# Kernel optimization log

Hardware: AMD Instinct MI355X
Metric: run time of the kernel (lower is better)

## Reference

```python
import jax, jax.numpy as jnp
import numpy as np

B, S, H, OUT = 4096, 200, 512, 64


def setup_inputs() -> dict:
    key = jax.random.key(0)
    ks = jax.random.split(key, 16)
    sc = 0.05
    return {
        "last_input": jax.random.normal(ks[0], (B, OUT), jnp.float32),
        "hidden": jax.random.normal(ks[1], (1, B, H), jnp.float32),
        "encoder_outputs": jax.random.normal(ks[2], (S, B, H), jnp.float32),
        "attn_W": jax.random.normal(ks[3], (S, H + OUT), jnp.float32) * sc,
        "attn_b": jax.random.normal(ks[4], (S,), jnp.float32) * sc,
        "comb_W": jax.random.normal(ks[5], (H, H + OUT), jnp.float32) * sc,
        "comb_b": jax.random.normal(ks[6], (H,), jnp.float32) * sc,
        "w_ih": jax.random.normal(ks[7], (3 * H, H), jnp.float32) * sc,
        "w_hh": jax.random.normal(ks[8], (3 * H, H), jnp.float32) * sc,
        "b_ih": jax.random.normal(ks[9], (3 * H,), jnp.float32) * sc,
        "b_hh": jax.random.normal(ks[10], (3 * H,), jnp.float32) * sc,
        "out_W": jax.random.normal(ks[11], (OUT, H), jnp.float32) * sc,
        "out_b": jax.random.normal(ks[12], (OUT,), jnp.float32) * sc,
    }


def reference(last_input, hidden, encoder_outputs, attn_W, attn_b, comb_W,
              comb_b, w_ih, w_hh, b_ih, b_hh, out_W, out_b):
    h0 = hidden[0]  # [B,H]
    # Bahdanau-style attention scores over the encoder sequence
    cat1 = jnp.concatenate([last_input, h0], axis=1)          # [B, OUT+H]
    attn_weights = jax.nn.softmax(cat1 @ attn_W.T + attn_b, axis=1)  # [B,S]
    enc = jnp.transpose(encoder_outputs, (1, 0, 2))            # [B,S,H]
    attn_applied = jnp.einsum('bs,bsh->bh', attn_weights, enc)  # [B,H]
    # combine + relu
    cat2 = jnp.concatenate([last_input, attn_applied], axis=1)  # [B, OUT+H]
    x = jax.nn.relu(cat2 @ comb_W.T + comb_b)                   # [B,H]
    # single-step GRU (PyTorch gate order: r, z, n)
    gi = x @ w_ih.T + b_ih                                      # [B,3H]
    gh = h0 @ w_hh.T + b_hh                                     # [B,3H]
    i_r, i_z, i_n = jnp.split(gi, 3, axis=1)
    h_r, h_z, h_n = jnp.split(gh, 3, axis=1)
    r = jax.nn.sigmoid(i_r + h_r)
    z = jax.nn.sigmoid(i_z + h_z)
    n = jnp.tanh(i_n + r * h_n)
    h_new = (1.0 - z) * n + z * h0                              # [B,H]
    out = h_new @ out_W.T + out_b                               # [B,OUT]
    return out, h_new[None], attn_weights
```

## Files before the change

kernel.cpp:

```cpp
#include <hip/hip_runtime.h>
#include <cstddef>

constexpr int Bn = 4096;
constexpr int Sn = 200;
constexpr int Hn = 512;
constexpr int On = 64;
constexpr int K1 = 576;

constexpr size_t HNEW_OFF = (size_t)Bn * On;
constexpr size_t AW_OFF   = (size_t)Bn * On + (size_t)Bn * Hn;

constexpr size_t CAT1B_OFF = 0;
constexpr size_t CAT2B_OFF = CAT1B_OFF + (size_t)Bn * K1 * 2;
constexpr size_t XB_OFF    = CAT2B_OFF + (size_t)Bn * K1 * 2;
constexpr size_t WIHB_OFF  = XB_OFF    + (size_t)Bn * Hn * 2;
constexpr size_t WHHB_OFF  = WIHB_OFF  + (size_t)3 * Hn * Hn * 2;
constexpr size_t CWB_OFF   = WHHB_OFF  + (size_t)3 * Hn * Hn * 2;
constexpr size_t OWB_OFF   = CWB_OFF   + (size_t)Hn * K1 * 2;
constexpr size_t AWB_OFF   = OWB_OFF   + (size_t)On * Hn * 2;
constexpr size_t HNB_OFF   = AWB_OFF   + (size_t)256 * K1 * 2;

typedef __attribute__((ext_vector_type(8))) short bf16x8;
typedef __attribute__((ext_vector_type(4))) float f32x4;

__device__ __forceinline__ float sigmoidf_(float v) { return 1.f / (1.f + __expf(-v)); }
__device__ __forceinline__ unsigned short f2bf(float f) {
    unsigned u = __float_as_uint(f);
    return (unsigned short)((u + 0x7FFFu + ((u >> 16) & 1u)) >> 16);
}
__device__ __forceinline__ ushort4 pack4(float4 v) {
    ushort4 o = { f2bf(v.x), f2bf(v.y), f2bf(v.z), f2bf(v.w) };
    return o;
}

__global__ __launch_bounds__(256) void cvt_all_kernel(
    const float* __restrict__ hidden, const float* __restrict__ wih,
    const float* __restrict__ whh, const float* __restrict__ combW,
    const float* __restrict__ outW, const float* __restrict__ attnW,
    const float* __restrict__ li,
    unsigned short* __restrict__ cat1b, unsigned short* __restrict__ cat2b,
    unsigned short* __restrict__ wihb, unsigned short* __restrict__ whhb,
    unsigned short* __restrict__ combWb, unsigned short* __restrict__ outWb,
    unsigned short* __restrict__ awWb)
{
    const int blk = blockIdx.x;
    const int t = threadIdx.x;
    if (blk < 2048) {
        size_t off = (size_t)blk * 1024 + (size_t)t * 4;
        int b = (int)(off >> 9), col = (int)(off & 511);
        float4 v = *(const float4*)(hidden + off);
        *(ushort4*)(cat1b + (size_t)b * K1 + On + col) = pack4(v);
    } else if (blk < 3584) {
        size_t off = (size_t)(blk - 2048) * 1024 + (size_t)t * 4;
        const float* s = (blk < 2816) ? wih : whh;
        unsigned short* d = (blk < 2816) ? wihb : whhb;
        if (blk >= 2816) off -= (size_t)768 * 1024;
        float4 v = *(const float4*)(s + off);
        *(ushort4*)(d + off) = pack4(v);
    } else if (blk < 3872) {
        size_t off = (size_t)(blk - 3584) * 1024 + (size_t)t * 4;
        float4 v = *(const float4*)(combW + off);
        *(ushort4*)(combWb + off) = pack4(v);
    } else if (blk < 3904) {
        size_t off = (size_t)(blk - 3872) * 1024 + (size_t)t * 4;
        float4 v = *(const float4*)(outW + off);
        *(ushort4*)(outWb + off) = pack4(v);
    } else if (blk < 4017) {
        size_t off = (size_t)(blk - 3904) * 1024 + (size_t)t * 4;
        if (off < (size_t)Sn * K1) {
            float4 v = *(const float4*)(attnW + off);
            *(ushort4*)(awWb + off) = pack4(v);
        }
    } else if (blk < 4049) {
        size_t off = (size_t)Sn * K1 + (size_t)(blk - 4017) * 1024 + (size_t)t * 4;
        if (off < (size_t)256 * K1) {
            ushort4 z = {0, 0, 0, 0};
            *(ushort4*)(awWb + off) = z;
        }
    } else {
        size_t off = (size_t)(blk - 4049) * 1024 + (size_t)t * 4;
        int b = (int)(off >> 6), col = (int)(off & 63);
        float4 v = *(const float4*)(li + off);
        ushort4 o = pack4(v);
        *(ushort4*)(cat1b + (size_t)b * K1 + col) = o;
        *(ushort4*)(cat2b + (size_t)b * K1 + col) = o;
    }
}

template<int MF, int NF, bool RELU, bool OUT_BF16>
__device__ __forceinline__ void gemm_bt_body(
    const unsigned short* __restrict__ A, int lda,
    const unsigned short* __restrict__ B,
    const float* __restrict__ bias, float* __restrict__ Cf,
    unsigned short* __restrict__ Cb, int K, int ldc,
    int m0, int n0, int nmax)
{
    constexpr int BM = 32 * MF;
    constexpr int BN = 32 * NF;
    __shared__ unsigned short As[BM * 64];
    __shared__ unsigned short Bs[BN * 64];

    const int tid = threadIdx.x;
    const int wave = tid >> 6;
    const int lane = tid & 63;
    const int wm = wave >> 1, wn = wave & 1;
    const int l15 = lane & 15, lg = lane >> 4;

    f32x4 acc[MF][NF];
#pragma unroll
    for (int i = 0; i < MF; ++i)
#pragma unroll
        for (int j = 0; j < NF; ++j) acc[i][j] = (f32x4){0.f, 0.f, 0.f, 0.f};

    for (int kc = 0; kc < K; kc += 64) {
        __syncthreads();
#pragma unroll
        for (int i = 0; i < BM * 8 / 256; ++i) {
            int idx = tid + i * 256;
            int row = idx >> 3, ck = idx & 7;
            uint4 v = *(const uint4*)(A + (size_t)(m0 + row) * lda + kc + ck * 8);
            int byte = row * 128 + ((ck * 16) ^ ((row & 7) << 4));
            *(uint4*)((char*)As + byte) = v;
        }
#pragma unroll
        for (int i = 0; i < BN * 8 / 256; ++i) {
            int idx = tid + i * 256;
            int row = idx >> 3, ck = idx & 7;
            uint4 v = *(const uint4*)(B + (size_t)(n0 + row) * K + kc + ck * 8);
            int byte = row * 128 + ((ck * 16) ^ ((row & 7) << 4));
            *(uint4*)((char*)Bs + byte) = v;
        }
        __syncthreads();
#pragma unroll
        for (int s = 0; s < 2; ++s) {
            bf16x8 af[MF], bfr[NF];
#pragma unroll
            for (int i = 0; i < MF; ++i) {
                int row = wm * (MF * 16) + i * 16 + l15;
                int byte = row * 128 + ((s * 64 + lg * 16) ^ ((row & 7) << 4));
                af[i] = *(const bf16x8*)((const char*)As + byte);
            }
#pragma unroll
            for (int j = 0; j < NF; ++j) {
                int row = wn * (NF * 16) + j * 16 + l15;
                int byte = row * 128 + ((s * 64 + lg * 16) ^ ((row & 7) << 4));
                bfr[j] = *(const bf16x8*)((const char*)Bs + byte);
            }
#pragma unroll
            for (int i = 0; i < MF; ++i)
#pragma unroll
                for (int j = 0; j < NF; ++j)
                    acc[i][j] = __builtin_amdgcn_mfma_f32_16x16x32_bf16(
                        af[i], bfr[j], acc[i][j], 0, 0, 0);
        }
    }

#pragma unroll
    for (int i = 0; i < MF; ++i) {
        int m = m0 + wm * (MF * 16) + i * 16 + lg * 4;
#pragma unroll
        for (int j = 0; j < NF; ++j) {
            int n = n0 + wn * (NF * 16) + j * 16 + l15;
            if (n < nmax) {
                float bv = bias[n];
#pragma unroll
                for (int r = 0; r < 4; ++r) {
                    float v = acc[i][j][r] + bv;
                    if (RELU) v = fmaxf(v, 0.f);
                    if (OUT_BF16) Cb[(size_t)(m + r) * ldc + n] = f2bf(v);
                    else          Cf[(size_t)(m + r) * ldc + n] = v;
                }
            }
        }
    }
}

__global__ __launch_bounds__(256, 2) void comb_gemm_kernel(
    const unsigned short* __restrict__ cat2b, const unsigned short* __restrict__ combWb,
    const float* __restrict__ comb_b, unsigned short* __restrict__ xb)
{
    gemm_bt_body<4, 4, true, true>(cat2b, K1, combWb, comb_b, nullptr, xb,
                                   K1, Hn, blockIdx.x * 128, blockIdx.y * 128, Hn);
}

__global__ __launch_bounds__(256, 2) void out_gemm_kernel(
    const unsigned short* __restrict__ hnewb, const unsigned short* __restrict__ outWb,
    const float* __restrict__ out_b, float* __restrict__ dout)
{
    gemm_bt_body<4, 2, false, false>(hnewb, Hn, outWb, out_b, dout, nullptr,
                                     Hn, On, blockIdx.x * 128, 0, On);
}

__global__ __launch_bounds__(256) void scores_softmax_kernel(
    const unsigned short* __restrict__ cat1b, const unsigned short* __restrict__ awWb,
    const float* __restrict__ attn_b, float* __restrict__ dout)
{
    __shared__ unsigned short As[64 * 64];
    __shared__ unsigned short Bs[256 * 64];
    __shared__ float smax[4][64];
    __shared__ float ssum[4][64];

    const int tid = threadIdx.x;
    const int m0 = blockIdx.x * 64;
    const int wave = tid >> 6;
    const int lane = tid & 63;
    const int l15 = lane & 15, lg = lane >> 4;

    f32x4 acc[4][4];
#pragma unroll
    for (int i = 0; i < 4; ++i)
#pragma unroll
        for (int j = 0; j < 4; ++j) acc[i][j] = (f32x4){0.f, 0.f, 0.f, 0.f};

    for (int kc = 0; kc < K1; kc += 64) {
        __syncthreads();
#pragma unroll
        for (int i = 0; i < 2; ++i) {
            int idx = tid + i * 256;
            int row = idx >> 3, ck = idx & 7;
            uint4 v = *(const uint4*)(cat1b + (size_t)(m0 + row) * K1 + kc + ck * 8);
            int byte = row * 128 + ((ck * 16) ^ ((row & 7) << 4));
            *(uint4*)((char*)As + byte) = v;
        }
#pragma unroll
        for (int i = 0; i < 8; ++i) {
            int idx = tid + i * 256;
            int row = idx >> 3, ck = idx & 7;
            uint4 v = *(const uint4*)(awWb + (size_t)row * K1 + kc + ck * 8);
            int byte = row * 128 + ((ck * 16) ^ ((row & 7) << 4));
            *(uint4*)((char*)Bs + byte) = v;
        }
        __syncthreads();
#pragma unroll
        for (int s = 0; s < 2; ++s) {
            bf16x8 af[4], bfr[4];
#pragma unroll
            for (int i = 0; i < 4; ++i) {
                int row = i * 16 + l15;
                int byte = row * 128 + ((s * 64 + lg * 16) ^ ((row & 7) << 4));
                af[i] = *(const bf16x8*)((const char*)As + byte);
            }
#pragma unroll
            for (int j = 0; j < 4; ++j) {
                int row = wave * 64 + j * 16 + l15;
                int byte = row * 128 + ((s * 64 + lg * 16) ^ ((row & 7) << 4));
                bfr[j] = *(const bf16x8*)((const char*)Bs + byte);
            }
#pragma unroll
            for (int i = 0; i < 4; ++i)
#pragma unroll
                for (int j = 0; j < 4; ++j)
                    acc[i][j] = __builtin_amdgcn_mfma_f32_16x16x32_bf16(
                        af[i], bfr[j], acc[i][j], 0, 0, 0);
        }
    }

#pragma unroll
    for (int i = 0; i < 4; ++i)
#pragma unroll
        for (int j = 0; j < 4; ++j) {
            int n = wave * 64 + j * 16 + l15;
            float bv = (n < Sn) ? attn_b[n] : 0.f;
#pragma unroll
            for (int r = 0; r < 4; ++r)
                acc[i][j][r] = (n < Sn) ? (acc[i][j][r] + bv) : -3.0e38f;
        }

#pragma unroll
    for (int i = 0; i < 4; ++i) {
#pragma unroll
        for (int r = 0; r < 4; ++r) {
            float mx = fmaxf(fmaxf(acc[i][0][r], acc[i][1][r]),
                             fmaxf(acc[i][2][r], acc[i][3][r]));
#pragma unroll
            for (int o = 8; o > 0; o >>= 1) mx = fmaxf(mx, __shfl_xor(mx, o, 64));
            if (l15 == 0) smax[wave][i * 16 + lg * 4 + r] = mx;
        }
    }
    __syncthreads();
#pragma unroll
    for (int i = 0; i < 4; ++i) {
#pragma unroll
        for (int r = 0; r < 4; ++r) {
            int row = i * 16 + lg * 4 + r;
            float mx = fmaxf(fmaxf(smax[0][row], smax[1][row]),
                             fmaxf(smax[2][row], smax[3][row]));
            float sum = 0.f;
#pragma unroll
            for (int j = 0; j < 4; ++j) {
                float e = __expf(acc[i][j][r] - mx);
                acc[i][j][r] = e;
                sum += e;
            }
#pragma unroll
            for (int o = 8; o > 0; o >>= 1) sum += __shfl_xor(sum, o, 64);
            if (l15 == 0) ssum[wave][row] = sum;
        }
    }
    __syncthreads();
#pragma unroll
    for (int i = 0; i < 4; ++i) {
#pragma unroll
        for (int r = 0; r < 4; ++r) {
            int row = i * 16 + lg * 4 + r;
            float inv = 1.f / (ssum[0][row] + ssum[1][row] + ssum[2][row] + ssum[3][row]);
#pragma unroll
            for (int j = 0; j < 4; ++j) {
                int n = wave * 64 + j * 16 + l15;
                if (n < Sn)
                    dout[AW_OFF + (size_t)(m0 + row) * Sn + n] = acc[i][j][r] * inv;
            }
        }
    }
}

__global__ __launch_bounds__(256) void attn_apply_kernel(
    const float* __restrict__ enc, const float* __restrict__ aw,
    unsigned short* __restrict__ cat2b)
{
    __shared__ float wl[2 * Sn];
    const int tid = threadIdx.x;
    const int b0 = blockIdx.x * 2;

    for (int idx = tid; idx < 2 * Sn; idx += 256)
        wl[idx] = aw[(size_t)b0 * Sn + idx];
    __syncthreads();

    const int r = tid >> 7;
    const int hc = tid & 127;
    const f32x4* base = (const f32x4*)enc + ((size_t)(b0 + r)) * 128 + hc;
    const float* w = &wl[r * Sn];

    f32x4 acc = {0, 0, 0, 0};
#pragma unroll 4
    for (int s = 0; s < Sn; ++s) {
        f32x4 v = __builtin_nontemporal_load(base + (size_t)s * (Bn * 128));
        acc += v * w[s];
    }

    ushort4 o = { f2bf(acc[0]), f2bf(acc[1]), f2bf(acc[2]), f2bf(acc[3]) };
    *(ushort4*)(cat2b + (size_t)(b0 + r) * K1 + On + hc * 4) = o;
}

__device__ __forceinline__ void gru_gemm_phase(
    const unsigned short* __restrict__ A, int lda,
    const unsigned short* __restrict__ W,
    int m0, int n0, int tid, int wm, int wn, int l15, int lg,
    unsigned short* As, unsigned short* Bs,
    f32x4 aR[2][2], f32x4 aZ[2][2], f32x4 aN[2][2])
{
    for (int kc = 0; kc < Hn; kc += 64) {
        __syncthreads();
#pragma unroll
        for (int i = 0; i < 2; ++i) {
            int idx = tid + i * 256;
            int row = idx >> 3, ck = idx & 7;
            uint4 v = *(const uint4*)(A + (size_t)(m0 + row) * lda + kc + ck * 8);
            int byte = row * 128 + ((ck * 16) ^ ((row & 7) << 4));
            *(uint4*)((char*)As + byte) = v;
        }
#pragma unroll
        for (int g = 0; g < 3; ++g)
#pragma unroll
            for (int i = 0; i < 2; ++i) {
                int idx = tid + i * 256;
                int row = idx >> 3, ck = idx & 7;
                uint4 v = *(const uint4*)(W + (size_t)(g * Hn + n0 + row) * Hn + kc + ck * 8);
                int byte = row * 128 + ((ck * 16) ^ ((row & 7) << 4));
                *(uint4*)((char*)Bs + g * 8192 + byte) = v;
            }
        __syncthreads();
#pragma unroll
        for (int s = 0; s < 2; ++s) {
            bf16x8 af[2], bf0[2], bf1[2], bf2[2];
#pragma unroll
            for (int i = 0; i < 2; ++i) {
                int row = wm * 32 + i * 16 + l15;
                int byte = row * 128 + ((s * 64 + lg * 16) ^ ((row & 7) << 4));
                af[i] = *(const bf16x8*)((const char*)As + byte);
            }
#pragma unroll
            for (int j = 0; j < 2; ++j) {
                int row = wn * 32 + j * 16 + l15;
                int byte = row * 128 + ((s * 64 + lg * 16) ^ ((row & 7) << 4));
                bf0[j] = *(const bf16x8*)((const char*)Bs + 0 * 8192 + byte);
                bf1[j] = *(const bf16x8*)((const char*)Bs + 1 * 8192 + byte);
                bf2[j] = *(const bf16x8*)((const char*)Bs + 2 * 8192 + byte);
            }
#pragma unroll
            for (int i = 0; i < 2; ++i)
#pragma unroll
                for (int j = 0; j < 2; ++j) {
                    aR[i][j] = __builtin_amdgcn_mfma_f32_16x16x32_bf16(af[i], bf0[j], aR[i][j], 0, 0, 0);
                    aZ[i][j] = __builtin_amdgcn_mfma_f32_16x16x32_bf16(af[i], bf1[j], aZ[i][j], 0, 0, 0);
                    aN[i][j] = __builtin_amdgcn_mfma_f32_16x16x32_bf16(af[i], bf2[j], aN[i][j], 0, 0, 0);
                }
        }
    }
}

__global__ __launch_bounds__(256, 2) void gru_fused_kernel(
    const unsigned short* __restrict__ xb, const unsigned short* __restrict__ cat1b,
    const unsigned short* __restrict__ wihb, const unsigned short* __restrict__ whhb,
    const float* __restrict__ b_ih, const float* __restrict__ b_hh,
    const float* __restrict__ hidden,
    float* __restrict__ dout, unsigned short* __restrict__ hnewb)
{
    __shared__ unsigned short As[64 * 64];
    __shared__ unsigned short Bs[3 * 64 * 64];

    const int tid = threadIdx.x;
    const int m0 = blockIdx.x * 64;
    const int n0 = blockIdx.y * 64;
    const int wave = tid >> 6, lane = tid & 63;
    const int wm = wave >> 1, wn = wave & 1;
    const int l15 = lane & 15, lg = lane >> 4;

    f32x4 aR[2][2], aZ[2][2], aN0[2][2], aN1[2][2];
#pragma unroll
    for (int i = 0; i < 2; ++i)
#pragma unroll
        for (int j = 0; j < 2; ++j) {
            aR[i][j] = (f32x4){0.f, 0.f, 0.f, 0.f};
            aZ[i][j] = (f32x4){0.f, 0.f, 0.f, 0.f};
            aN0[i][j] = (f32x4){0.f, 0.f, 0.f, 0.f};
            aN1[i][j] = (f32x4){0.f, 0.f, 0.f, 0.f};
        }

    gru_gemm_phase(xb, Hn, wihb, m0, n0, tid, wm, wn, l15, lg, As, Bs, aR, aZ, aN0);
    gru_gemm_phase(cat1b + On, K1, whhb, m0, n0, tid, wm, wn, l15, lg, As, Bs, aR, aZ, aN1);

#pragma unroll
    for (int j = 0; j < 2; ++j) {
        const int n = n0 + wn * 32 + j * 16 + l15;
        const float bR = b_ih[n] + b_hh[n];
        const float bZ = b_ih[Hn + n] + b_hh[Hn + n];
        const float bI = b_ih[2 * Hn + n];
        const float bH = b_hh[2 * Hn + n];
#pragma unroll
        for (int i = 0; i < 2; ++i) {
            const int mb = m0 + wm * 32 + i * 16 + lg * 4;
#pragma unroll
            for (int r = 0; r < 4; ++r) {
                const int m = mb + r;
                float h0 = hidden[(size_t)m * Hn + n];
                float rg = sigmoidf_(aR[i][j][r] + bR);
                float zg = sigmoidf_(aZ[i][j][r] + bZ);
                float ng = tanhf(aN0[i][j][r] + bI + rg * (aN1[i][j][r] + bH));
                float o = (1.f - zg) * ng + zg * h0;
                dout[HNEW_OFF + (size_t)m * Hn + n] = o;
                hnewb[(size_t)m * Hn + n] = f2bf(o);
            }
        }
    }
}

extern "C" void kernel_launch(void* const* d_in, const int* in_sizes, int n_in,
                              void* d_out, int out_size, void* d_ws, size_t ws_size,
                              hipStream_t stream)
{
    const float* last_input = (const float*)d_in[0];
    const float* hidden     = (const float*)d_in[1];
    const float* enc        = (const float*)d_in[2];
    const float* attn_W     = (const float*)d_in[3];
    const float* attn_b     = (const float*)d_in[4];
    const float* comb_W     = (const float*)d_in[5];
    const float* comb_b     = (const float*)d_in[6];
    const float* w_ih       = (const float*)d_in[7];
    const float* w_hh       = (const float*)d_in[8];
    const float* b_ih       = (const float*)d_in[9];
    const float* b_hh       = (const float*)d_in[10];
    const float* out_W      = (const float*)d_in[11];
    const float* out_b      = (const float*)d_in[12];

    float* out = (float*)d_out;
    char*  ws  = (char*)d_ws;
    unsigned short* cat1b  = (unsigned short*)(ws + CAT1B_OFF);
    unsigned short* cat2b  = (unsigned short*)(ws + CAT2B_OFF);
    unsigned short* xb     = (unsigned short*)(ws + XB_OFF);
    unsigned short* wihb   = (unsigned short*)(ws + WIHB_OFF);
    unsigned short* whhb   = (unsigned short*)(ws + WHHB_OFF);
    unsigned short* combWb = (unsigned short*)(ws + CWB_OFF);
    unsigned short* outWb  = (unsigned short*)(ws + OWB_OFF);
    unsigned short* awWb   = (unsigned short*)(ws + AWB_OFF);
    unsigned short* hnewb  = (unsigned short*)(ws + HNB_OFF);

    cvt_all_kernel<<<4305, 256, 0, stream>>>(hidden, w_ih, w_hh, comb_W, out_W,
                                             attn_W, last_input,
                                             cat1b, cat2b, wihb, whhb, combWb,
                                             outWb, awWb);
    scores_softmax_kernel<<<Bn / 64, 256, 0, stream>>>(cat1b, awWb, attn_b, out);
    attn_apply_kernel<<<Bn / 2, 256, 0, stream>>>(enc, out + AW_OFF, cat2b);
    comb_gemm_kernel<<<dim3(Bn / 128, Hn / 128), 256, 0, stream>>>(cat2b, combWb, comb_b, xb);
    gru_fused_kernel<<<dim3(Bn / 64, Hn / 64), 256, 0, stream>>>(
        xb, cat1b, wihb, whhb, b_ih, b_hh, hidden, out, hnewb);
    out_gemm_kernel<<<Bn / 128, 256, 0, stream>>>(hnewb, outWb, out_b, out);
}
```

Measured before the change: 374.6 us.

## Fuse fp32-to-bf16 conversion into GEMM tile loads and drop pre-conversion kernel

Removes the separate conversion kernel that wrote bf16 copies of hidden, weights and concatenated inputs to workspace. Each GEMM now reads fp32 sources directly and converts to bf16 while staging tiles into shared memory, and the concatenations are handled by switching source pointer on the first K chunk. The attention-apply kernel now processes 8 batch rows per block with four accumulators per thread. This saves a launch and the round trip through workspace, but weights are re-read and re-converted in fp32 by every block, which doubles global load bytes for the weight tiles.

```diff
diff --git a/kernel.cpp b/kernel.cpp
--- a/kernel.cpp
+++ b/kernel.cpp
@@ -10,15 +10,9 @@
 constexpr size_t HNEW_OFF = (size_t)Bn * On;
 constexpr size_t AW_OFF   = (size_t)Bn * On + (size_t)Bn * Hn;
 
-constexpr size_t CAT1B_OFF = 0;
-constexpr size_t CAT2B_OFF = CAT1B_OFF + (size_t)Bn * K1 * 2;
-constexpr size_t XB_OFF    = CAT2B_OFF + (size_t)Bn * K1 * 2;
-constexpr size_t WIHB_OFF  = XB_OFF    + (size_t)Bn * Hn * 2;
-constexpr size_t WHHB_OFF  = WIHB_OFF  + (size_t)3 * Hn * Hn * 2;
-constexpr size_t CWB_OFF   = WHHB_OFF  + (size_t)3 * Hn * Hn * 2;
-constexpr size_t OWB_OFF   = CWB_OFF   + (size_t)Hn * K1 * 2;
-constexpr size_t AWB_OFF   = OWB_OFF   + (size_t)On * Hn * 2;
-constexpr size_t HNB_OFF   = AWB_OFF   + (size_t)256 * K1 * 2;
+constexpr size_t ATTNA_OFF = 0;
+constexpr size_t XB_OFF    = ATTNA_OFF + (size_t)Bn * Hn * 2;
+constexpr size_t HNB_OFF   = XB_OFF    + (size_t)Bn * Hn * 2;
 
 typedef __attribute__((ext_vector_type(8))) short bf16x8;
 typedef __attribute__((ext_vector_type(4))) float f32x4;
@@ -28,172 +22,21 @@
     unsigned u = __float_as_uint(f);
     return (unsigned short)((u + 0x7FFFu + ((u >> 16) & 1u)) >> 16);
 }
-__device__ __forceinline__ ushort4 pack4(float4 v) {
-    ushort4 o = { f2bf(v.x), f2bf(v.y), f2bf(v.z), f2bf(v.w) };
-    return o;
-}
-
-__global__ __launch_bounds__(256) void cvt_all_kernel(
-    const float* __restrict__ hidden, const float* __restrict__ wih,
-    const float* __restrict__ whh, const float* __restrict__ combW,
-    const float* __restrict__ outW, const float* __restrict__ attnW,
-    const float* __restrict__ li,
-    unsigned short* __restrict__ cat1b, unsigned short* __restrict__ cat2b,
-    unsigned short* __restrict__ wihb, unsigned short* __restrict__ whhb,
-    unsigned short* __restrict__ combWb, unsigned short* __restrict__ outWb,
-    unsigned short* __restrict__ awWb)
-{
-    const int blk = blockIdx.x;
-    const int t = threadIdx.x;
-    if (blk < 2048) {
-        size_t off = (size_t)blk * 1024 + (size_t)t * 4;
-        int b = (int)(off >> 9), col = (int)(off & 511);
-        float4 v = *(const float4*)(hidden + off);
-        *(ushort4*)(cat1b + (size_t)b * K1 + On + col) = pack4(v);
-    } else if (blk < 3584) {
-        size_t off = (size_t)(blk - 2048) * 1024 + (size_t)t * 4;
-        const float* s = (blk < 2816) ? wih : whh;
-        unsigned short* d = (blk < 2816) ? wihb : whhb;
-        if (blk >= 2816) off -= (size_t)768 * 1024;
-        float4 v = *(const float4*)(s + off);
-        *(ushort4*)(d + off) = pack4(v);
-    } else if (blk < 3872) {
-        size_t off = (size_t)(blk - 3584) * 1024 + (size_t)t * 4;
-        float4 v = *(const float4*)(combW + off);
-        *(ushort4*)(combWb + off) = pack4(v);
-    } else if (blk < 3904) {
-        size_t off = (size_t)(blk - 3872) * 1024 + (size_t)t * 4;
-        float4 v = *(const float4*)(outW + off);
-        *(ushort4*)(outWb + off) = pack4(v);
-    } else if (blk < 4017) {
-        size_t off = (size_t)(blk - 3904) * 1024 + (size_t)t * 4;
-        if (off < (size_t)Sn * K1) {
-            float4 v = *(const float4*)(attnW + off);
-            *(ushort4*)(awWb + off) = pack4(v);
-        }
-    } else if (blk < 4049) {
-        size_t off = (size_t)Sn * K1 + (size_t)(blk - 4017) * 1024 + (size_t)t * 4;
-        if (off < (size_t)256 * K1) {
-            ushort4 z = {0, 0, 0, 0};
-            *(ushort4*)(awWb + off) = z;
-        }
-    } else {
-        size_t off = (size_t)(blk - 4049) * 1024 + (size_t)t * 4;
-        int b = (int)(off >> 6), col = (int)(off & 63);
-        float4 v = *(const float4*)(li + off);
-        ushort4 o = pack4(v);
-        *(ushort4*)(cat1b + (size_t)b * K1 + col) = o;
-        *(ushort4*)(cat2b + (size_t)b * K1 + col) = o;
-    }
-}
-
-template<int MF, int NF, bool RELU, bool OUT_BF16>
-__device__ __forceinline__ void gemm_bt_body(
-    const unsigned short* __restrict__ A, int lda,
-    const unsigned short* __restrict__ B,
-    const float* __restrict__ bias, float* __restrict__ Cf,
-    unsigned short* __restrict__ Cb, int K, int ldc,
-    int m0, int n0, int nmax)
-{
-    constexpr int BM = 32 * MF;
-    constexpr int BN = 32 * NF;
-    __shared__ unsigned short As[BM * 64];
-    __shared__ unsigned short Bs[BN * 64];
-
-    const int tid = threadIdx.x;
-    const int wave = tid >> 6;
-    const int lane = tid & 63;
-    const int wm = wave >> 1, wn = wave & 1;
-    const int l15 = lane & 15, lg = lane >> 4;
-
-    f32x4 acc[MF][NF];
-#pragma unroll
-    for (int i = 0; i < MF; ++i)
-#pragma unroll
-        for (int j = 0; j < NF; ++j) acc[i][j] = (f32x4){0.f, 0.f, 0.f, 0.f};
-
-    for (int kc = 0; kc < K; kc += 64) {
-        __syncthreads();
-#pragma unroll
-        for (int i = 0; i < BM * 8 / 256; ++i) {
-            int idx = tid + i * 256;
-            int row = idx >> 3, ck = idx & 7;
-            uint4 v = *(const uint4*)(A + (size_t)(m0 + row) * lda + kc + ck * 8);
-            int byte = row * 128 + ((ck * 16) ^ ((row & 7) << 4));
-            *(uint4*)((char*)As + byte) = v;
-        }
-#pragma unroll
-        for (int i = 0; i < BN * 8 / 256; ++i) {
-            int idx = tid + i * 256;
-            int row = idx >> 3, ck = idx & 7;
-            uint4 v = *(const uint4*)(B + (size_t)(n0 + row) * K + kc + ck * 8);
-            int byte = row * 128 + ((ck * 16) ^ ((row & 7) << 4));
-            *(uint4*)((char*)Bs + byte) = v;
-        }
-        __syncthreads();
-#pragma unroll
-        for (int s = 0; s < 2; ++s) {
-            bf16x8 af[MF], bfr[NF];
-#pragma unroll
-            for (int i = 0; i < MF; ++i) {
-                int row = wm * (MF * 16) + i * 16 + l15;
-                int byte = row * 128 + ((s * 64 + lg * 16) ^ ((row & 7) << 4));
-                af[i] = *(const bf16x8*)((const char*)As + byte);
-            }
-#pragma unroll
-            for (int j = 0; j < NF; ++j) {
-                int row = wn * (NF * 16) + j * 16 + l15;
-                int byte = row * 128 + ((s * 64 + lg * 16) ^ ((row & 7) << 4));
-                bfr[j] = *(const bf16x8*)((const char*)Bs + byte);
-            }
-#pragma unroll
-            for (int i = 0; i < MF; ++i)
-#pragma unroll
-                for (int j = 0; j < NF; ++j)
-                    acc[i][j] = __builtin_amdgcn_mfma_f32_16x16x32_bf16(
-                        af[i], bfr[j], acc[i][j], 0, 0, 0);
-        }
-    }
-
-#pragma unroll
-    for (int i = 0; i < MF; ++i) {
-        int m = m0 + wm * (MF * 16) + i * 16 + lg * 4;
-#pragma unroll
-        for (int j = 0; j < NF; ++j) {
-            int n = n0 + wn * (NF * 16) + j * 16 + l15;
-            if (n < nmax) {
-                float bv = bias[n];
-#pragma unroll
-                for (int r = 0; r < 4; ++r) {
-                    float v = acc[i][j][r] + bv;
-                    if (RELU) v = fmaxf(v, 0.f);
-                    if (OUT_BF16) Cb[(size_t)(m + r) * ldc + n] = f2bf(v);
-                    else          Cf[(size_t)(m + r) * ldc + n] = v;
-                }
-            }
-        }
-    }
-}
-
-__global__ __launch_bounds__(256, 2) void comb_gemm_kernel(
-    const unsigned short* __restrict__ cat2b, const unsigned short* __restrict__ combWb,
-    const float* __restrict__ comb_b, unsigned short* __restrict__ xb)
-{
-    gemm_bt_body<4, 4, true, true>(cat2b, K1, combWb, comb_b, nullptr, xb,
-                                   K1, Hn, blockIdx.x * 128, blockIdx.y * 128, Hn);
-}
-
-__global__ __launch_bounds__(256, 2) void out_gemm_kernel(
-    const unsigned short* __restrict__ hnewb, const unsigned short* __restrict__ outWb,
-    const float* __restrict__ out_b, float* __restrict__ dout)
-{
-    gemm_bt_body<4, 2, false, false>(hnewb, Hn, outWb, out_b, dout, nullptr,
-                                     Hn, On, blockIdx.x * 128, 0, On);
+__device__ __forceinline__ uint4 cvt8(const float* p) {
+    float4 a = *(const float4*)p;
+    float4 b = *(const float4*)(p + 4);
+    uint4 r;
+    r.x = (unsigned)f2bf(a.x) | ((unsigned)f2bf(a.y) << 16);
+    r.y = (unsigned)f2bf(a.z) | ((unsigned)f2bf(a.w) << 16);
+    r.z = (unsigned)f2bf(b.x) | ((unsigned)f2bf(b.y) << 16);
+    r.w = (unsigned)f2bf(b.z) | ((unsigned)f2bf(b.w) << 16);
+    return r;
 }
 
 __global__ __launch_bounds__(256) void scores_softmax_kernel(
-    const unsigned short* __restrict__ cat1b, const unsigned short* __restrict__ awWb,
-    const float* __restrict__ attn_b, float* __restrict__ dout)
+    const float* __restrict__ li, const float* __restrict__ hidden,
+    const float* __restrict__ attnW, const float* __restrict__ attn_b,
+    float* __restrict__ dout)
 {
     __shared__ unsigned short As[64 * 64];
     __shared__ unsigned short Bs[256 * 64];
@@ -218,7 +61,10 @@
         for (int i = 0; i < 2; ++i) {
             int idx = tid + i * 256;
             int row = idx >> 3, ck = idx & 7;
-            uint4 v = *(const uint4*)(cat1b + (size_t)(m0 + row) * K1 + kc + ck * 8);
+            const float* src = (kc == 0)
+                ? (li + (size_t)(m0 + row) * On + ck * 8)
+                : (hidden + (size_t)(m0 + row) * Hn + (kc - 64) + ck * 8);
+            uint4 v = cvt8(src);
             int byte = row * 128 + ((ck * 16) ^ ((row & 7) << 4));
             *(uint4*)((char*)As + byte) = v;
         }
@@ -226,7 +72,8 @@
         for (int i = 0; i < 8; ++i) {
             int idx = tid + i * 256;
             int row = idx >> 3, ck = idx & 7;
-            uint4 v = *(const uint4*)(awWb + (size_t)row * K1 + kc + ck * 8);
+            uint4 v = {0, 0, 0, 0};
+            if (row < Sn) v = cvt8(attnW + (size_t)row * K1 + kc + ck * 8);
             int byte = row * 128 + ((ck * 16) ^ ((row & 7) << 4));
             *(uint4*)((char*)Bs + byte) = v;
         }
@@ -316,35 +163,132 @@
 
 __global__ __launch_bounds__(256) void attn_apply_kernel(
     const float* __restrict__ enc, const float* __restrict__ aw,
-    unsigned short* __restrict__ cat2b)
-{
-    __shared__ float wl[2 * Sn];
+    unsigned short* __restrict__ attnA)
+{
+    __shared__ float wl[8 * Sn];
     const int tid = threadIdx.x;
-    const int b0 = blockIdx.x * 2;
-
-    for (int idx = tid; idx < 2 * Sn; idx += 256)
+    const int b0 = blockIdx.x * 8;
+
+    for (int idx = tid; idx < 8 * Sn; idx += 256)
         wl[idx] = aw[(size_t)b0 * Sn + idx];
     __syncthreads();
 
-    const int r = tid >> 7;
+    const int q = tid >> 7;
     const int hc = tid & 127;
-    const f32x4* base = (const f32x4*)enc + ((size_t)(b0 + r)) * 128 + hc;
-    const float* w = &wl[r * Sn];
-
-    f32x4 acc = {0, 0, 0, 0};
-#pragma unroll 4
+    const f32x4* base = (const f32x4*)enc + ((size_t)(b0 + q * 4)) * 128 + hc;
+
+    f32x4 a0 = {0,0,0,0}, a1 = {0,0,0,0}, a2 = {0,0,0,0}, a3 = {0,0,0,0};
+
+#pragma unroll 2
     for (int s = 0; s < Sn; ++s) {
-        f32x4 v = __builtin_nontemporal_load(base + (size_t)s * (Bn * 128));
-        acc += v * w[s];
-    }
-
-    ushort4 o = { f2bf(acc[0]), f2bf(acc[1]), f2bf(acc[2]), f2bf(acc[3]) };
-    *(ushort4*)(cat2b + (size_t)(b0 + r) * K1 + On + hc * 4) = o;
-}
-
+        const f32x4* p = base + (size_t)s * (Bn * 128);
+        f32x4 v0 = __builtin_nontemporal_load(p);
+        f32x4 v1 = __builtin_nontemporal_load(p + 128);
+        f32x4 v2 = __builtin_nontemporal_load(p + 256);
+        f32x4 v3 = __builtin_nontemporal_load(p + 384);
+        float w0 = wl[(q * 4 + 0) * Sn + s];
+        float w1 = wl[(q * 4 + 1) * Sn + s];
+        float w2 = wl[(q * 4 + 2) * Sn + s];
+        float w3 = wl[(q * 4 + 3) * Sn + s];
+        a0 += v0 * w0; a1 += v1 * w1; a2 += v2 * w2; a3 += v3 * w3;
+    }
+
+    const int h = hc * 4;
+    f32x4 accs[4] = {a0, a1, a2, a3};
+#pragma unroll
+    for (int r = 0; r < 4; ++r) {
+        ushort4 o = { f2bf(accs[r][0]), f2bf(accs[r][1]), f2bf(accs[r][2]), f2bf(accs[r][3]) };
+        *(ushort4*)(attnA + (size_t)(b0 + q * 4 + r) * Hn + h) = o;
+    }
+}
+
+__global__ __launch_bounds__(256, 2) void comb_gemm_kernel(
+    const float* __restrict__ li, const unsigned short* __restrict__ attnA,
+    const float* __restrict__ combW, const float* __restrict__ comb_b,
+    unsigned short* __restrict__ xb)
+{
+    __shared__ unsigned short As[128 * 64];
+    __shared__ unsigned short Bs[128 * 64];
+
+    const int tid = threadIdx.x;
+    const int m0 = blockIdx.x * 128;
+    const int n0 = blockIdx.y * 128;
+    const int wave = tid >> 6, lane = tid & 63;
+    const int wm = wave >> 1, wn = wave & 1;
+    const int l15 = lane & 15, lg = lane >> 4;
+
+    f32x4 acc[4][4];
+#pragma unroll
+    for (int i = 0; i < 4; ++i)
+#pragma unroll
+        for (int j = 0; j < 4; ++j) acc[i][j] = (f32x4){0.f, 0.f, 0.f, 0.f};
+
+    for (int kc = 0; kc < K1; kc += 64) {
+        __syncthreads();
+#pragma unroll
+        for (int i = 0; i < 4; ++i) {
+            int idx = tid + i * 256;
+            int row = idx >> 3, ck = idx & 7;
+            uint4 v;
+            if (kc == 0)
+                v = cvt8(li + (size_t)(m0 + row) * On + ck * 8);
+            else
+                v = *(const uint4*)(attnA + (size_t)(m0 + row) * Hn + (kc - 64) + ck * 8);
+            int byte = row * 128 + ((ck * 16) ^ ((row & 7) << 4));
+            *(uint4*)((char*)As + byte) = v;
+        }
+#pragma unroll
+        for (int i = 0; i < 4; ++i) {
+            int idx = tid + i * 256;
+            int row = idx >> 3, ck = idx & 7;
+            uint4 v = cvt8(combW + (size_t)(n0 + row) * K1 + kc + ck * 8);
+            int byte = row * 128 + ((ck * 16) ^ ((row & 7) << 4));
+            *(uint4*)((char*)Bs + byte) = v;
+        }
+        __syncthreads();
+#pragma unroll
+        for (int s = 0; s < 2; ++s) {
+            bf16x8 af[4], bfr[4];
+#pragma unroll
+            for (int i = 0; i < 4; ++i) {
+                int row = wm * 64 + i * 16 + l15;
+                int byte = row * 128 + ((s * 64 + lg * 16) ^ ((row & 7) << 4));
+                af[i] = *(const bf16x8*)((const char*)As + byte);
+            }
+#pragma unroll
+            for (int j = 0; j < 4; ++j) {
+                int row = wn * 64 + j * 16 + l15;
+                int byte = row * 128 + ((s * 64 + lg * 16) ^ ((row & 7) << 4));
+                bfr[j] = *(const bf16x8*)((const char*)Bs + byte);
+            }
+#pragma unroll
+            for (int i = 0; i < 4; ++i)
+#pragma unroll
+                for (int j = 0; j < 4; ++j)
+                    acc[i][j] = __builtin_amdgcn_mfma_f32_16x16x32_bf16(
+                        af[i], bfr[j], acc[i][j], 0, 0, 0);
+        }
+    }
+
+#pragma unroll
+    for (int i = 0; i < 4; ++i) {
+        int m = m0 + wm * 64 + i * 16 + lg * 4;
+#pragma unroll
+        for (int j = 0; j < 4; ++j) {
+            int n = n0 + wn * 64 + j * 16 + l15;
+            float bv = comb_b[n];
+#pragma unroll
+            for (int r = 0; r < 4; ++r) {
+                float v = fmaxf(acc[i][j][r] + bv, 0.f);
+                xb[(size_t)(m + r) * Hn + n] = f2bf(v);
+            }
+        }
+    }
+}
+
+template<bool AF32>
 __device__ __forceinline__ void gru_gemm_phase(
-    const unsigned short* __restrict__ A, int lda,
-    const unsigned short* __restrict__ W,
+    const void* __restrict__ A, const float* __restrict__ W,
     int m0, int n0, int tid, int wm, int wn, int l15, int lg,
     unsigned short* As, unsigned short* Bs,
     f32x4 aR[2][2], f32x4 aZ[2][2], f32x4 aN[2][2])
@@ -355,7 +299,11 @@
         for (int i = 0; i < 2; ++i) {
             int idx = tid + i * 256;
             int row = idx >> 3, ck = idx & 7;
-            uint4 v = *(const uint4*)(A + (size_t)(m0 + row) * lda + kc + ck * 8);
+            uint4 v;
+            if (AF32)
+                v = cvt8((const float*)A + (size_t)(m0 + row) * Hn + kc + ck * 8);
+            else
+                v = *(const uint4*)((const unsigned short*)A + (size_t)(m0 + row) * Hn + kc + ck * 8);
             int byte = row * 128 + ((ck * 16) ^ ((row & 7) << 4));
             *(uint4*)((char*)As + byte) = v;
         }
@@ -365,7 +313,7 @@
             for (int i = 0; i < 2; ++i) {
                 int idx = tid + i * 256;
                 int row = idx >> 3, ck = idx & 7;
-                uint4 v = *(const uint4*)(W + (size_t)(g * Hn + n0 + row) * Hn + kc + ck * 8);
+                uint4 v = cvt8(W + (size_t)(g * Hn + n0 + row) * Hn + kc + ck * 8);
                 int byte = row * 128 + ((ck * 16) ^ ((row & 7) << 4));
                 *(uint4*)((char*)Bs + g * 8192 + byte) = v;
             }
@@ -400,10 +348,9 @@
 }
 
 __global__ __launch_bounds__(256, 2) void gru_fused_kernel(
-    const unsigned short* __restrict__ xb, const unsigned short* __restrict__ cat1b,
-    const unsigned short* __restrict__ wihb, const unsigned short* __restrict__ whhb,
+    const unsigned short* __restrict__ xb, const float* __restrict__ hidden,
+    const float* __restrict__ wih, const float* __restrict__ whh,
     const float* __restrict__ b_ih, const float* __restrict__ b_hh,
-    const float* __restrict__ hidden,
     float* __restrict__ dout, unsigned short* __restrict__ hnewb)
 {
     __shared__ unsigned short As[64 * 64];
@@ -427,8 +374,8 @@
             aN1[i][j] = (f32x4){0.f, 0.f, 0.f, 0.f};
         }
 
-    gru_gemm_phase(xb, Hn, wihb, m0, n0, tid, wm, wn, l15, lg, As, Bs, aR, aZ, aN0);
-    gru_gemm_phase(cat1b + On, K1, whhb, m0, n0, tid, wm, wn, l15, lg, As, Bs, aR, aZ, aN1);
+    gru_gemm_phase<false>(xb, wih, m0, n0, tid, wm, wn, l15, lg, As, Bs, aR, aZ, aN0);
+    gru_gemm_phase<true>(hidden, whh, m0, n0, tid, wm, wn, l15, lg, As, Bs, aR, aZ, aN1);
 
 #pragma unroll
     for (int j = 0; j < 2; ++j) {
@@ -451,6 +398,82 @@
                 dout[HNEW_OFF + (size_t)m * Hn + n] = o;
                 hnewb[(size_t)m * Hn + n] = f2bf(o);
             }
+        }
+    }
+}
+
+__global__ __launch_bounds__(256, 2) void out_gemm_kernel(
+    const unsigned short* __restrict__ hnewb, const float* __restrict__ outW,
+    const float* __restrict__ out_b, float* __restrict__ dout)
+{
+    __shared__ unsigned short As[128 * 64];
+    __shared__ unsigned short Bs[64 * 64];
+
+    const int tid = threadIdx.x;
+    const int m0 = blockIdx.x * 128;
+    const int wave = tid >> 6, lane = tid & 63;
+    const int wm = wave >> 1, wn = wave & 1;
+    const int l15 = lane & 15, lg = lane >> 4;
+
+    f32x4 acc[4][2];
+#pragma unroll
+    for (int i = 0; i < 4; ++i)
+#pragma unroll
+        for (int j = 0; j < 2; ++j) acc[i][j] = (f32x4){0.f, 0.f, 0.f, 0.f};
+
+    for (int kc = 0; kc < Hn; kc += 64) {
+        __syncthreads();
+#pragma unroll
+        for (int i = 0; i < 4; ++i) {
+            int idx = tid + i * 256;
+            int row = idx >> 3, ck = idx & 7;
+            uint4 v = *(const uint4*)(hnewb + (size_t)(m0 + row) * Hn + kc + ck * 8);
+            int byte = row * 128 + ((ck * 16) ^ ((row & 7) << 4));
+            *(uint4*)((char*)As + byte) = v;
+        }
+#pragma unroll
+        for (int i = 0; i < 2; ++i) {
+            int idx = tid + i * 256;
+            int row = idx >> 3, ck = idx & 7;
+            uint4 v = cvt8(outW + (size_t)row * Hn + kc + ck * 8);
+            int byte = row * 128 + ((ck * 16) ^ ((row & 7) << 4));
+            *(uint4*)((char*)Bs + byte) = v;
+        }
+        __syncthreads();
+#pragma unroll
+        for (int s = 0; s < 2; ++s) {
+            bf16x8 af[4], bfr[2];
+#pragma unroll
+            for (int i = 0; i < 4; ++i) {
+                int row = wm * 64 + i * 16 + l15;
+                int byte = row * 128 + ((s * 64 + lg * 16) ^ ((row & 7) << 4));
+                af[i] = *(const bf16x8*)((const char*)As + byte);
+            }
+#pragma unroll
+            for (int j = 0; j < 2; ++j) {
+                int row = wn * 32 + j * 16 + l15;
+                int byte = row * 128 + ((s * 64 + lg * 16) ^ ((row & 7) << 4));
+                bfr[j] = *(const bf16x8*)((const char*)Bs + byte);
+            }
+#pragma unroll
+            for (int i = 0; i < 4; ++i)
+#pragma unroll
+                for (int j = 0; j < 2; ++j)
+                    acc[i][j] = __builtin_amdgcn_mfma_f32_16x16x32_bf16(
+                        af[i], bfr[j], acc[i][j], 0, 0, 0);
+        }
+    }
+
+#pragma unroll
+    for (int i = 0; i < 4; ++i) {
+        int m = m0 + wm * 64 + i * 16 + lg * 4;
+#pragma unroll
+        for (int j = 0; j < 2; ++j) {
+            int n = wn * 32 + j * 16 + l15;
+            float bv = out_b[n];
+#pragma unroll
+            for (int r = 0; r < 4; ++r)
+                dout[(size_t)(m + r) * On + n] = acc[i][j][r] + bv;
         }
     }
 }
@@ -475,24 +498,16 @@
 
     float* out = (float*)d_out;
     char*  ws  = (char*)d_ws;
-    unsigned short* cat1b  = (unsigned short*)(ws + CAT1B_OFF);
-    unsigned short* cat2b  = (unsigned short*)(ws + CAT2B_OFF);
-    unsigned short* xb     = (unsigned short*)(ws + XB_OFF);
-    unsigned short* wihb   = (unsigned short*)(ws + WIHB_OFF);
-    unsigned short* whhb   = (unsigned short*)(ws + WHHB_OFF);
-    unsigned short* combWb = (unsigned short*)(ws + CWB_OFF);
-    unsigned short* outWb  = (unsigned short*)(ws + OWB_OFF);
-    unsigned short* awWb   = (unsigned short*)(ws + AWB_OFF);
-    unsigned short* hnewb  = (unsigned short*)(ws + HNB_OFF);
-
-    cvt_all_kernel<<<4305, 256, 0, stream>>>(hidden, w_ih, w_hh, comb_W, out_W,
-                                             attn_W, last_input,
-                                             cat1b, cat2b, wihb, whhb, combWb,
-                                             outWb, awWb);
-    scores_softmax_kernel<<<Bn / 64, 256, 0, stream>>>(cat1b, awWb, attn_b, out);
-    attn_apply_kernel<<<Bn / 2, 256, 0, stream>>>(enc, out + AW_OFF, cat2b);
-    comb_gemm_kernel<<<dim3(Bn / 128, Hn / 128), 256, 0, stream>>>(cat2b, combWb, comb_b, xb);
+    unsigned short* attnA = (unsigned short*)(ws + ATTNA_OFF);
+    unsigned short* xb    = (unsigned short*)(ws + XB_OFF);
+    unsigned short* hnewb = (unsigned short*)(ws + HNB_OFF);
+
+    scores_softmax_kernel<<<Bn / 64, 256, 0, stream>>>(last_input, hidden, attn_W,
+                                                       attn_b, out);
+    attn_apply_kernel<<<Bn / 8, 256, 0, stream>>>(enc, out + AW_OFF, attnA);
+    comb_gemm_kernel<<<dim3(Bn / 128, Hn / 128), 256, 0, stream>>>(
+        last_input, attnA, comb_W, comb_b, xb);
     gru_fused_kernel<<<dim3(Bn / 64, Hn / 64), 256, 0, stream>>>(
-        xb, cat1b, wihb, whhb, b_ih, b_hh, hidden, out, hnewb);
-    out_gemm_kernel<<<Bn / 128, 256, 0, stream>>>(hnewb, outWb, out_b, out);
-}
+        xb, hidden, w_ih, w_hh, b_ih, b_hh, out, hnewb);
+    out_gemm_kernel<<<Bn / 128, 256, 0, stream>>>(hnewb, out_W, out_b, out);
+}
```

Result: slower. 385.1 us (+2.8%).
